# Performance work log

Measured on AMD Instinct MI355X. Metric: run time of the kernel, lower is better.

The kernel has to match this reference:

```python
import jax, jax.numpy as jnp
import numpy as np

B, T, I, H, O = 32, 128, 256, 512, 10


def setup_inputs() -> dict:
    key = jax.random.key(0)
    ks = jax.random.split(key, 16)
    s = 1.0 / np.sqrt(H)
    si = 1.0 / np.sqrt(I)
    inp = {
        "x": jax.random.normal(ks[0], (B, T, I), jnp.float32),
        # LSTM params (gate order: i, f, g, o)
        "Wih": jax.random.uniform(ks[1], (4 * H, I), jnp.float32, -si, si),
        "Whh": jax.random.uniform(ks[2], (4 * H, H), jnp.float32, -s, s),
        "b_lstm": jax.random.uniform(ks[3], (4 * H,), jnp.float32, -s, s),
        # readout dense
        "Wd": jax.random.uniform(ks[4], (O, H), jnp.float32, -s, s),
        "bd": jnp.zeros((O,), jnp.float32),
        # synthetic gradient MLP: H -> 512 -> 256 -> 128 -> H
        "Ws1": jax.random.uniform(ks[5], (512, H), jnp.float32, -s, s),
        "bs1": jnp.zeros((512,), jnp.float32),
        "Ws2": jax.random.uniform(ks[6], (256, 512), jnp.float32, -1.0 / np.sqrt(512), 1.0 / np.sqrt(512)),
        "bs2": jnp.zeros((256,), jnp.float32),
        "Ws3": jax.random.uniform(ks[7], (128, 256), jnp.float32, -1.0 / np.sqrt(256), 1.0 / np.sqrt(256)),
        "bs3": jnp.zeros((128,), jnp.float32),
        "Ws4": jax.random.uniform(ks[8], (H, 128), jnp.float32, -1.0 / np.sqrt(128), 1.0 / np.sqrt(128)),
        "bs4": jnp.zeros((H,), jnp.float32),
    }
    return inp


def reference(x, Wih, Whh, b_lstm, Wd, bd, Ws1, bs1, Ws2, bs2, Ws3, bs3, Ws4, bs4):
    # batch_first: [B,T,I] -> [T,B,I]
    xs = jnp.swapaxes(x, 0, 1)
    b, hid = x.shape[0], Whh.shape[1]

    h0 = jnp.zeros((b, hid), x.dtype)
    c0 = jnp.zeros((b, hid), x.dtype)
    # e-prop eligibility vectors: one row per (gate in {i,f,g}) x hidden unit
    ev_x0 = jnp.zeros((b, 3 * hid, Wih.shape[1]), x.dtype)
    ev_h0 = jnp.zeros((b, 3 * hid, hid), x.dtype)
    ev_b0 = jnp.zeros((b, 3 * hid, 1), x.dtype)

    def step(carry, xt):
        h, c, ev_x, ev_h, ev_b = carry
        gates = xt @ Wih.T + h @ Whh.T + b_lstm  # [B,4H]
        gi, gf, gg, go = jnp.split(gates, 4, axis=1)
        i = jax.nn.sigmoid(gi)
        f = jax.nn.sigmoid(gf)
        g = jnp.tanh(gg)
        o = jax.nn.sigmoid(go)
        # d(c_t)/d(pre-activation) for cell-affecting gates i, f, g  -> [B,3H]
        d = jnp.concatenate([g * i * (1.0 - i),
                             c * f * (1.0 - f),
                             i * (1.0 - g * g)], axis=1)
        f3 = jnp.concatenate([f, f, f], axis=1)  # forget-gate decay, tiled per gate
        # eligibility trace outer-product updates (the memory-bound core)
        ev_x_n = ev_x * f3[:, :, None] + d[:, :, None] * xt[:, None, :]
        ev_h_n = ev_h * f3[:, :, None] + d[:, :, None] * h[:, None, :]
        ev_b_n = ev_b * f3[:, :, None] + d[:, :, None]
        c_n = f * c + i * g
        h_n = o * jnp.tanh(c_n)
        return (h_n, c_n, ev_x_n, ev_h_n, ev_b_n), h_n

    (hT, cT, ev_x, ev_h, ev_b), hs = jax.lax.scan(step, (h0, c0, ev_x0, ev_h0, ev_b0), xs)

    last = hs[-1]  # [B,H]
    # synthetic gradient MLP on last hidden state
    z = jax.nn.relu(last @ Ws1.T + bs1)
    z = jax.nn.relu(z @ Ws2.T + bs2)
    z = jax.nn.relu(z @ Ws3.T + bs3)
    synth_grad = z @ Ws4.T + bs4  # [B,H]
    # readout on last hidden state (single_output=True)
    predictions = last @ Wd.T + bd  # [B,O]
    return (predictions, synth_grad, ev_x, ev_h, ev_b)
```

## Files before the change

kernel.cpp:

```cpp
#include <hip/hip_runtime.h>


typedef __attribute__((ext_vector_type(8))) short short8;
typedef __attribute__((ext_vector_type(4))) float f32x4;
typedef __attribute__((ext_vector_type(4))) unsigned u32x4;

#define DEV static __device__ __forceinline__

DEV unsigned f2bf(float x) {
  union { float f; unsigned u; } v; v.f = x;
  return (v.u + 0x7fffu + ((v.u >> 16) & 1u)) >> 16;
}
DEV float bf2f(unsigned b) {
  union { float f; unsigned u; } v; v.u = b << 16;
  return v.f;
}
struct HiLo { unsigned hi, lo; };
DEV HiLo packpair(float a, float b) {
  unsigned ha = f2bf(a), hb = f2bf(b);
  unsigned la = f2bf(a - bf2f(ha)), lb = f2bf(b - bf2f(hb));
  HiLo r; r.hi = ha | (hb << 16); r.lo = la | (lb << 16);
  return r;
}

#define SENT 0x7F7F7F7Fu

__global__ __launch_bounds__(1024) void lstm_rec(
    const float* __restrict__ Whh,
    const float* __restrict__ XW,
    unsigned* __restrict__ Hp,
    float* __restrict__ Hf,
    float* __restrict__ dh,
    float* __restrict__ fh)
{
  const int wg   = blockIdx.x;
  const int tid  = threadIdx.x;
  const int lane = tid & 63;
  const int wave = tid >> 6;
  const int tM   = wave & 1;
  const int tN   = wave >> 1;

  __shared__ __align__(16) unsigned Ldh[32 * 256];
  __shared__ float gl[32][132];

  const int cc = lane & 15;
  const int kb = lane >> 4;

  const int rloc  = tN * 16 + cc;
  const int jglob = (rloc >> 5) * 512 + wg * 32 + (rloc & 31);
  short8 whi[16];
#pragma unroll
  for (int s = 0; s < 16; ++s) {
    const float* wp = Whh + (size_t)jglob * 512 + s * 32 + kb * 8;
    f32x4 w0 = *(const f32x4*)wp;
    f32x4 w1 = *(const f32x4*)(wp + 4);
    short8 hi;
#pragma unroll
    for (int j = 0; j < 4; ++j) {
      hi[j]     = (short)f2bf(w0[j]);
      hi[4 + j] = (short)f2bf(w1[j]);
    }
    whi[s] = hi;
  }

  const int bA = tM * 16 + cc;
  const int mz = bA & 7;
  const unsigned rbase = (unsigned)(bA * 256 + ((kb ^ (mz & 3)) << 2) + ((mz >> 2) << 4));

  const int beW  = lane >> 1;
  const int half = lane & 1;
  const int swz  = beW & 7;
  const int C0   = wave * 4 + half * 2;

  const int be = tid >> 5;
  const int jo = tid & 31;
  const int jh = wg * 32 + jo;
  float c_reg = 0.f;

  for (int t = 0; t < 128; ++t) {
    const float* xwp = XW + (size_t)t * 65536 + (size_t)be * 2048 + wg * 32 + jo;
    float xwi = xwp[0], xwf = xwp[512], xwg = xwp[1024], xwo = xwp[1536];

    if (t > 0) {
      const unsigned* sp = Hp + ((size_t)t * 16 + wave) * 512 + lane * 8;
      u32x4 h0, h1;
      for (;;) {
#define SLICE_LOAD(dst, addr)                                          \
        asm volatile("global_load_dwordx4 %0, %1, off sc0 sc1"         \
                     : "=&v"(dst) : "v"(addr) : "memory")
        SLICE_LOAD(h0, sp);
        SLICE_LOAD(h1, sp + 4);
#undef SLICE_LOAD
        asm volatile("s_waitcnt vmcnt(0)" ::: "memory");
        __builtin_amdgcn_sched_barrier(0);
        unsigned bad = (unsigned)((h0[0] == SENT) | (h0[1] == SENT) |
                                  (h0[2] == SENT) | (h0[3] == SENT) |
                                  (h1[0] == SENT) | (h1[1] == SENT) |
                                  (h1[2] == SENT) | (h1[3] == SENT));
        if (!__any((int)bad)) break;
        __builtin_amdgcn_s_sleep(1);
      }
      __builtin_amdgcn_sched_barrier(0);

      const unsigned wb = (unsigned)(beW * 256);
      *(u32x4*)&Ldh[wb + (((C0 + 0) ^ swz) << 2)] = h0;
      *(u32x4*)&Ldh[wb + (((C0 + 1) ^ swz) << 2)] = h1;
    }
    __syncthreads();

    f32x4 acc;
    {
      f32x4 a0 = {0.f, 0.f, 0.f, 0.f}, a1 = a0;
      if (t > 0) {
#pragma unroll
        for (int s = 0; s < 16; s += 2) {
          const unsigned i0 = rbase ^ (unsigned)(s << 4);
          const unsigned i1 = rbase ^ (unsigned)((s + 1) << 4);
          short8 ah0 = __builtin_bit_cast(short8, *(const u32x4*)&Ldh[i0]);
          short8 ah1 = __builtin_bit_cast(short8, *(const u32x4*)&Ldh[i1]);
          a0 = __builtin_amdgcn_mfma_f32_16x16x32_bf16(ah0, whi[s],     a0, 0, 0, 0);
          a1 = __builtin_amdgcn_mfma_f32_16x16x32_bf16(ah1, whi[s + 1], a1, 0, 0, 0);
        }
      }
      acc = a0 + a1;
    }
#pragma unroll
    for (int r = 0; r < 4; ++r)
      gl[tM * 16 + kb * 4 + r][tN * 16 + cc] = acc[r];
    __syncthreads();

    {
      float pi = xwi + gl[be][jo];
      float pf = xwf + gl[be][32 + jo];
      float pg = xwg + gl[be][64 + jo];
      float po = xwo + gl[be][96 + jo];
      float ig = 1.f / (1.f + expf(-pi));
      float fg = 1.f / (1.f + expf(-pf));
      float gg = tanhf(pg);
      float og = 1.f / (1.f + expf(-po));
      float di = gg * ig * (1.f - ig);
      float df = c_reg * fg * (1.f - fg);
      float dg = ig * (1.f - gg * gg);
      c_reg = fg * c_reg + ig * gg;
      float hn = og * tanhf(c_reg);

      unsigned hh = f2bf(hn);
      unsigned hh_nb = (unsigned)__shfl_xor((int)hh, 1);
      if (!(jo & 1)) {
        unsigned stv = hh | (hh_nb << 16);
        size_t sa = ((size_t)(t + 1) * 16 + wg) * 512 + be * 16 + (jo >> 1);
        __hip_atomic_store(&Hp[sa], stv, __ATOMIC_RELAXED, __HIP_MEMORY_SCOPE_AGENT);
      }

      Hf[(size_t)(t + 1) * 16384 + (size_t)be * 512 + jh] = hn;
      size_t db = (size_t)t * 49152 + (size_t)be * 1536 + jh;
      dh[db] = di; dh[db + 512] = df; dh[db + 1024] = dg;
      fh[(size_t)t * 16384 + (size_t)be * 512 + jh] = fg;
    }
  }
}

__global__ __launch_bounds__(256) void suffix_A(
    float* __restrict__ dh, const float* __restrict__ fh,
    float* __restrict__ evb)
{
  const int g = blockIdx.x * 256 + threadIdx.x;
  const int b = g >> 9, jh = g & 511;
  float F = 1.f, s0 = 0.f, s1 = 0.f, s2 = 0.f;
  for (int t = 127; t >= 0; --t) {
    size_t db = (size_t)t * 49152 + (size_t)b * 1536 + jh;
    float a0 = dh[db] * F, a1 = dh[db + 512] * F, a2 = dh[db + 1024] * F;
    dh[db] = a0; dh[db + 512] = a1; dh[db + 1024] = a2;
    s0 += a0; s1 += a1; s2 += a2;
    F *= fh[(size_t)t * 16384 + (size_t)b * 512 + jh];
  }
  size_t eb = (size_t)b * 1536 + jh;
  evb[eb] = s0; evb[eb + 512] = s1; evb[eb + 1024] = s2;
}

__global__ __launch_bounds__(256, 2) void gemm_bf16s(
    const float* __restrict__ A, const float* __restrict__ B,
    float* __restrict__ C, const float* __restrict__ bias,
    int M, int N, int K,
    long long sAm, long long sAk, long long aBatch,
    long long sBn, long long sBk, long long bBatch,
    long long sCm1, long long sCm2, int M1, long long cBatch)
{
  __shared__ __align__(16) unsigned Ahi[128 * 20], Alo[128 * 20];
  __shared__ __align__(16) unsigned Bhi[128 * 20], Blo[128 * 20];

  const int tid  = threadIdx.x;
  const int lane = tid & 63;
  const int wave = tid >> 6;
  const int wm   = wave >> 1;
  const int wn   = wave & 1;
  const int cc   = lane & 15;
  const int kb   = lane >> 4;
  const long long z = blockIdx.z;
  const float* Ab = A + z * aBatch;
  const float* Bb = B + z * bBatch;
  const int m0 = blockIdx.y * 128, n0 = blockIdx.x * 128;

  f32x4 acc[4][4];
#pragma unroll
  for (int i = 0; i < 4; ++i)
#pragma unroll
    for (int j = 0; j < 4; ++j) acc[i][j] = (f32x4){0.f, 0.f, 0.f, 0.f};

  for (int k0 = 0; k0 < K; k0 += 32) {
    if (sAk == 1) {
      const int r = tid >> 1, half = tid & 1;
      const float* s = Ab + (long long)(m0 + r) * sAm + (k0 + half * 16);
      f32x4 v0 = *(const f32x4*)s;
      f32x4 v1 = *(const f32x4*)(s + 4);
      f32x4 v2 = *(const f32x4*)(s + 8);
      f32x4 v3 = *(const f32x4*)(s + 12);
      u32x4 h0, h1, l0, l1;
      HiLo p;
      p = packpair(v0[0], v0[1]); h0[0] = p.hi; l0[0] = p.lo;
      p = packpair(v0[2], v0[3]); h0[1] = p.hi; l0[1] = p.lo;
      p = packpair(v1[0], v1[1]); h0[2] = p.hi; l0[2] = p.lo;
      p = packpair(v1[2], v1[3]); h0[3] = p.hi; l0[3] = p.lo;
      p = packpair(v2[0], v2[1]); h1[0] = p.hi; l1[0] = p.lo;
      p = packpair(v2[2], v2[3]); h1[1] = p.hi; l1[1] = p.lo;
      p = packpair(v3[0], v3[1]); h1[2] = p.hi; l1[2] = p.lo;
      p = packpair(v3[2], v3[3]); h1[3] = p.hi; l1[3] = p.lo;
      const int o = r * 20 + half * 8;
      *(u32x4*)&Ahi[o] = h0;  *(u32x4*)&Ahi[o + 4] = h1;
      *(u32x4*)&Alo[o] = l0;  *(u32x4*)&Alo[o + 4] = l1;
    } else {
#pragma unroll
      for (int it = 0; it < 2; ++it) {
        const int kp = tid >> 4;
        const int mr = (tid & 15) * 4 + it * 64;
        const float* s0 = Ab + (long long)(k0 + 2 * kp) * sAk + (m0 + mr);
        f32x4 va = *(const f32x4*)s0;
        f32x4 vb = *(const f32x4*)(s0 + sAk);
#pragma unroll
        for (int q = 0; q < 4; ++q) {
          HiLo p = packpair(va[q], vb[q]);
          Ahi[(mr + q) * 20 + kp] = p.hi;
          Alo[(mr + q) * 20 + kp] = p.lo;
        }
      }
    }
    if (sBk == 1) {
      const int r = tid >> 1, half = tid & 1;
      const float* s = Bb + (long long)(n0 + r) * sBn + (k0 + half * 16);
      f32x4 v0 = *(const f32x4*)s;
      f32x4 v1 = *(const f32x4*)(s + 4);
      f32x4 v2 = *(const f32x4*)(s + 8);
      f32x4 v3 = *(const f32x4*)(s + 12);
      u32x4 h0, h1, l0, l1;
      HiLo p;
      p = packpair(v0[0], v0[1]); h0[0] = p.hi; l0[0] = p.lo;
      p = packpair(v0[2], v0[3]); h0[1] = p.hi; l0[1] = p.lo;
      p = packpair(v1[0], v1[1]); h0[2] = p.hi; l0[2] = p.lo;
      p = packpair(v1[2], v1[3]); h0[3] = p.hi; l0[3] = p.lo;
      p = packpair(v2[0], v2[1]); h1[0] = p.hi; l1[0] = p.lo;
      p = packpair(v2[2], v2[3]); h1[1] = p.hi; l1[1] = p.lo;
      p = packpair(v3[0], v3[1]); h1[2] = p.hi; l1[2] = p.lo;
      p = packpair(v3[2], v3[3]); h1[3] = p.hi; l1[3] = p.lo;
      const int o = r * 20 + half * 8;
      *(u32x4*)&Bhi[o] = h0;  *(u32x4*)&Bhi[o + 4] = h1;
      *(u32x4*)&Blo[o] = l0;  *(u32x4*)&Blo[o + 4] = l1;
    } else {
#pragma unroll
      for (int it = 0; it < 2; ++it) {
        const int kp = tid >> 4;
        const int nr = (tid & 15) * 4 + it * 64;
        const float* s0 = Bb + (long long)(k0 + 2 * kp) * sBk + (n0 + nr);
        f32x4 va = *(const f32x4*)s0;
        f32x4 vb = *(const f32x4*)(s0 + sBk);
#pragma unroll
        for (int q = 0; q < 4; ++q) {
          HiLo p = packpair(va[q], vb[q]);
          Bhi[(nr + q) * 20 + kp] = p.hi;
          Blo[(nr + q) * 20 + kp] = p.lo;
        }
      }
    }
    __syncthreads();

    short8 ah[4], al[4], bh[4], bl[4];
#pragma unroll
    for (int mi = 0; mi < 4; ++mi) {
      const int row = wm * 64 + mi * 16 + cc;
      ah[mi] = __builtin_bit_cast(short8, *(const u32x4*)&Ahi[row * 20 + kb * 4]);
      al[mi] = __builtin_bit_cast(short8, *(const u32x4*)&Alo[row * 20 + kb * 4]);
    }
#pragma unroll
    for (int ni = 0; ni < 4; ++ni) {
      const int row = wn * 64 + ni * 16 + cc;
      bh[ni] = __builtin_bit_cast(short8, *(const u32x4*)&Bhi[row * 20 + kb * 4]);
      bl[ni] = __builtin_bit_cast(short8, *(const u32x4*)&Blo[row * 20 + kb * 4]);
    }
#pragma unroll
    for (int mi = 0; mi < 4; ++mi)
#pragma unroll
      for (int ni = 0; ni < 4; ++ni) {
        acc[mi][ni] = __builtin_amdgcn_mfma_f32_16x16x32_bf16(ah[mi], bh[ni], acc[mi][ni], 0, 0, 0);
        acc[mi][ni] = __builtin_amdgcn_mfma_f32_16x16x32_bf16(ah[mi], bl[ni], acc[mi][ni], 0, 0, 0);
        acc[mi][ni] = __builtin_amdgcn_mfma_f32_16x16x32_bf16(al[mi], bh[ni], acc[mi][ni], 0, 0, 0);
      }
    __syncthreads();
  }

#pragma unroll
  for (int ni = 0; ni < 4; ++ni) {
    const int ng = n0 + wn * 64 + ni * 16 + cc;
    const float bv = bias ? bias[ng] : 0.f;
#pragma unroll
    for (int mi = 0; mi < 4; ++mi) {
#pragma unroll
      for (int r = 0; r < 4; ++r) {
        const int mg = m0 + wm * 64 + mi * 16 + kb * 4 + r;
        const long long crow = z * cBatch + (long long)(mg % M1) * sCm1 +
                               (long long)(mg / M1) * sCm2;
        C[crow + ng] = acc[mi][ni][r] + bv;
      }
    }
  }
}

template <int BM, int BN, int TM, int TN>
__global__ __launch_bounds__(256) void gemm_f32(
    const float* __restrict__ A, const float* __restrict__ B,
    float* __restrict__ C, const float* __restrict__ bias,
    int M, int N, int K,
    long long sAm, long long sAk, long long aBatch,
    long long sBn, long long sBk, long long bBatch,
    long long sCm1, long long sCm2, int M1, long long cBatch,
    int relu)
{
  constexpr int BK = 16;
  __shared__ float As[BK][BM + 4];
  __shared__ float Bs[BK][BN + 4];
  const int tid = threadIdx.x;
  const long long z = blockIdx.z;
  const float* Ab = A + z * aBatch;
  const float* Bb = B + z * bBatch;
  const int m0 = blockIdx.y * BM, n0 = blockIdx.x * BN;
  constexpr int tn_cnt = BN / TN;
  const int tm0 = (tid / tn_cnt) * TM;
  const int tn0 = (tid % tn_cnt) * TN;

  float acc[TM][TN];
#pragma unroll
  for (int i = 0; i < TM; ++i)
#pragma unroll
    for (int j = 0; j < TN; ++j) acc[i][j] = 0.f;

  for (int k0 = 0; k0 < K; k0 += BK) {
    if (sAk == 1) {
      for (int m = tid >> 2; m < BM; m += 64) {
        const int kq = (tid & 3) * 4;
        f32x4 v = {0.f, 0.f, 0.f, 0.f};
        if (m0 + m < M) v = *(const f32x4*)(Ab + (long long)(m0 + m) * sAm + (k0 + kq));
        As[kq + 0][m] = v[0]; As[kq + 1][m] = v[1];
        As[kq + 2][m] = v[2]; As[kq + 3][m] = v[3];
      }
    } else {
      constexpr int mq_cnt = BM / 4;
      for (int kk = tid / mq_cnt; kk < BK; kk += 256 / mq_cnt) {
        const int mq = (tid % mq_cnt) * 4;
        f32x4 v = {0.f, 0.f, 0.f, 0.f};
        if (m0 + mq < M) v = *(const f32x4*)(Ab + (long long)(k0 + kk) * sAk + (m0 + mq));
        *(f32x4*)&As[kk][mq] = v;
      }
    }
    if (sBk == 1) {
      for (int n = tid >> 2; n < BN; n += 64) {
        const int kq = (tid & 3) * 4;
        f32x4 v = {0.f, 0.f, 0.f, 0.f};
        if (n0 + n < N) v = *(const f32x4*)(Bb + (long long)(n0 + n) * sBn + (k0 + kq));
        Bs[kq + 0][n] = v[0]; Bs[kq + 1][n] = v[1];
        Bs[kq + 2][n] = v[2]; Bs[kq + 3][n] = v[3];
      }
    } else {
      constexpr int nq_cnt = BN / 4;
      for (int kk = tid / nq_cnt; kk < BK; kk += 256 / nq_cnt) {
        const int nq = (tid % nq_cnt) * 4;
        f32x4 v = {0.f, 0.f, 0.f, 0.f};
        if (n0 + nq < N) v = *(const f32x4*)(Bb + (long long)(k0 + kk) * sBk + (n0 + nq));
        *(f32x4*)&Bs[kk][nq] = v;
      }
    }
    __syncthreads();

#pragma unroll
    for (int kk = 0; kk < BK; ++kk) {
      float a[TM], bb[TN];
#pragma unroll
      for (int i = 0; i < TM; ++i) a[i] = As[kk][tm0 + i];
#pragma unroll
      for (int j = 0; j < TN; ++j) bb[j] = Bs[kk][tn0 + j];
#pragma unroll
      for (int i = 0; i < TM; ++i)
#pragma unroll
        for (int j = 0; j < TN; ++j) acc[i][j] += a[i] * bb[j];
    }
    __syncthreads();
  }

#pragma unroll
  for (int i = 0; i < TM; ++i) {
    const int mg = m0 + tm0 + i;
    if (mg >= M) continue;
    const long long crow = z * cBatch + (long long)(mg % M1) * sCm1 +
                           (long long)(mg / M1) * sCm2;
#pragma unroll
    for (int j = 0; j < TN; ++j) {
      const int ng = n0 + tn0 + j;
      if (ng >= N) continue;
      float v = acc[i][j];
      if (bias) v += bias[ng];
      if (relu) v = fmaxf(v, 0.f);
      C[crow + ng] = v;
    }
  }
}

extern "C" void kernel_launch(void* const* d_in, const int* in_sizes, int n_in,
                              void* d_out, int out_size, void* d_ws, size_t ws_size,
                              hipStream_t stream) {
  const float* x   = (const float*)d_in[0];
  const float* Wih = (const float*)d_in[1];
  const float* Whh = (const float*)d_in[2];
  const float* bl  = (const float*)d_in[3];
  const float* Wd  = (const float*)d_in[4];
  const float* bd  = (const float*)d_in[5];
  const float* Ws1 = (const float*)d_in[6];
  const float* bs1 = (const float*)d_in[7];
  const float* Ws2 = (const float*)d_in[8];
  const float* bs2 = (const float*)d_in[9];
  const float* Ws3 = (const float*)d_in[10];
  const float* bs3 = (const float*)d_in[11];
  const float* Ws4 = (const float*)d_in[12];
  const float* bs4 = (const float*)d_in[13];

  float* out = (float*)d_out;
  float* ws  = (float*)d_ws;

  const long long OP = 0, OS = 320, OEX = 16704, OEH = 12599616, OEB = 37765440;

  float* XW = out + OEH;
  float* fh = out + OEH + 8388608;
  unsigned* Hp = (unsigned*)(out + OEH + 10485760);

  float* dh = ws;
  float* Hf = ws + 6291456;
  float* z1 = ws + 8404992;
  float* z2 = ws + 8421376;
  float* z3 = ws + 8429568;

  hipMemsetAsync(Hp, 0x7F, 129ull * 16 * 512 * sizeof(unsigned), stream);
  hipMemsetAsync(Hf, 0, 16384 * sizeof(float), stream);

  dim3 blk(256);

  gemm_bf16s<<<dim3(16, 32, 1), blk, 0, stream>>>(
      x, Wih, XW, bl, 4096, 2048, 256,
      256, 1, 0,
      256, 1, 0,
      65536, 2048, 128, 0);

  lstm_rec<<<dim3(16), dim3(1024), 0, stream>>>(Whh, XW, Hp, Hf, dh, fh);

  suffix_A<<<dim3(64), blk, 0, stream>>>(dh, fh, out + OEB);

  const float* hlast = Hf + 2097152;
  gemm_f32<32, 32, 2, 2><<<dim3(16, 1, 1), blk, 0, stream>>>(
      hlast, Ws1, z1, bs1, 32, 512, 512, 512, 1, 0, 512, 1, 0, 512, 0, 32, 0, 1);
  gemm_f32<32, 32, 2, 2><<<dim3(8, 1, 1), blk, 0, stream>>>(
      z1, Ws2, z2, bs2, 32, 256, 512, 512, 1, 0, 512, 1, 0, 256, 0, 32, 0, 1);
  gemm_f32<32, 32, 2, 2><<<dim3(4, 1, 1), blk, 0, stream>>>(
      z2, Ws3, z3, bs3, 32, 128, 256, 256, 1, 0, 256, 1, 0, 128, 0, 32, 0, 1);
  gemm_f32<32, 32, 2, 2><<<dim3(16, 1, 1), blk, 0, stream>>>(
      z3, Ws4, out + OS, bs4, 32, 512, 128, 128, 1, 0, 128, 1, 0, 512, 0, 32, 0, 0);
  gemm_f32<32, 32, 2, 2><<<dim3(1, 1, 1), blk, 0, stream>>>(
      hlast, Wd, out + OP, bd, 32, 10, 512, 512, 1, 0, 512, 1, 0, 10, 0, 32, 0, 0);

  gemm_bf16s<<<dim3(2, 12, 32), blk, 0, stream>>>(
      dh, x, out + OEX, nullptr, 1536, 256, 128,
      1, 49152, 1536,
      1, 256, 32768,
      256, 0, 1536, 393216);

  gemm_bf16s<<<dim3(4, 12, 32), blk, 0, stream>>>(
      dh, Hf, out + OEH, nullptr, 1536, 512, 128,
      1, 49152, 1536,
      1, 16384, 512,
      512, 0, 1536, 786432);
}
```

Baseline: 775.9 us.

## Halve LSTM recurrence block size, give each wave two gate tiles

Result: faster. 677.8 us (-12.6%).

```diff
diff --git a/kernel.cpp b/kernel.cpp
--- a/kernel.cpp
+++ b/kernel.cpp
@@ -2,6 +2,7 @@
 
 
 typedef __attribute__((ext_vector_type(8))) short short8;
+typedef __attribute__((ext_vector_type(2))) float f32x2;
 typedef __attribute__((ext_vector_type(4))) float f32x4;
 typedef __attribute__((ext_vector_type(4))) unsigned u32x4;
 
@@ -25,7 +26,7 @@
 
 #define SENT 0x7F7F7F7Fu
 
-__global__ __launch_bounds__(1024) void lstm_rec(
+__global__ __launch_bounds__(512, 2) void lstm_rec(
     const float* __restrict__ Whh,
     const float* __restrict__ XW,
     unsigned* __restrict__ Hp,
@@ -46,21 +47,24 @@
   const int cc = lane & 15;
   const int kb = lane >> 4;
 
-  const int rloc  = tN * 16 + cc;
-  const int jglob = (rloc >> 5) * 512 + wg * 32 + (rloc & 31);
-  short8 whi[16];
-#pragma unroll
-  for (int s = 0; s < 16; ++s) {
-    const float* wp = Whh + (size_t)jglob * 512 + s * 32 + kb * 8;
-    f32x4 w0 = *(const f32x4*)wp;
-    f32x4 w1 = *(const f32x4*)(wp + 4);
-    short8 hi;
-#pragma unroll
-    for (int j = 0; j < 4; ++j) {
-      hi[j]     = (short)f2bf(w0[j]);
-      hi[4 + j] = (short)f2bf(w1[j]);
-    }
-    whi[s] = hi;
+  short8 whiA[16], whiB[16];
+#pragma unroll
+  for (int q = 0; q < 2; ++q) {
+    const int rloc  = (tN * 2 + q) * 16 + cc;
+    const int jglob = (rloc >> 5) * 512 + wg * 32 + (rloc & 31);
+#pragma unroll
+    for (int s = 0; s < 16; ++s) {
+      const float* wp = Whh + (size_t)jglob * 512 + s * 32 + kb * 8;
+      f32x4 w0 = *(const f32x4*)wp;
+      f32x4 w1 = *(const f32x4*)(wp + 4);
+      short8 hi;
+#pragma unroll
+      for (int j = 0; j < 4; ++j) {
+        hi[j]     = (short)f2bf(w0[j]);
+        hi[4 + j] = (short)f2bf(w1[j]);
+      }
+      if (q == 0) whiA[s] = hi; else whiB[s] = hi;
+    }
   }
 
   const int bA = tM * 16 + cc;
@@ -70,92 +74,100 @@
   const int beW  = lane >> 1;
   const int half = lane & 1;
   const int swz  = beW & 7;
-  const int C0   = wave * 4 + half * 2;
-
-  const int be = tid >> 5;
-  const int jo = tid & 31;
-  const int jh = wg * 32 + jo;
-  float c_reg = 0.f;
+  const int Ca   = 4 * (wave * 2)     + half * 2;
+  const int Cb   = 4 * (wave * 2 + 1) + half * 2;
+
+  const int be  = tid >> 4;
+  const int jo0 = (tid & 15) * 2;
+  const int jh0 = wg * 32 + jo0;
+  float c0 = 0.f, c1 = 0.f;
 
   for (int t = 0; t < 128; ++t) {
-    const float* xwp = XW + (size_t)t * 65536 + (size_t)be * 2048 + wg * 32 + jo;
-    float xwi = xwp[0], xwf = xwp[512], xwg = xwp[1024], xwo = xwp[1536];
+    const float* xwp = XW + (size_t)t * 65536 + (size_t)be * 2048 + wg * 32 + jo0;
+    f32x2 xwi = *(const f32x2*)(xwp);
+    f32x2 xwf = *(const f32x2*)(xwp + 512);
+    f32x2 xwg = *(const f32x2*)(xwp + 1024);
+    f32x2 xwo = *(const f32x2*)(xwp + 1536);
 
     if (t > 0) {
-      const unsigned* sp = Hp + ((size_t)t * 16 + wave) * 512 + lane * 8;
-      u32x4 h0, h1;
+      const unsigned* sp0 = Hp + ((size_t)t * 16 + wave * 2) * 512 + lane * 8;
+      const unsigned* sp1 = sp0 + 512;
+      u32x4 a0, a1, b0, b1;
       for (;;) {
 #define SLICE_LOAD(dst, addr)                                          \
         asm volatile("global_load_dwordx4 %0, %1, off sc0 sc1"         \
                      : "=&v"(dst) : "v"(addr) : "memory")
-        SLICE_LOAD(h0, sp);
-        SLICE_LOAD(h1, sp + 4);
+        SLICE_LOAD(a0, sp0);
+        SLICE_LOAD(a1, sp0 + 4);
+        SLICE_LOAD(b0, sp1);
+        SLICE_LOAD(b1, sp1 + 4);
 #undef SLICE_LOAD
         asm volatile("s_waitcnt vmcnt(0)" ::: "memory");
         __builtin_amdgcn_sched_barrier(0);
-        unsigned bad = (unsigned)((h0[0] == SENT) | (h0[1] == SENT) |
-                                  (h0[2] == SENT) | (h0[3] == SENT) |
-                                  (h1[0] == SENT) | (h1[1] == SENT) |
-                                  (h1[2] == SENT) | (h1[3] == SENT));
+        unsigned bad = (unsigned)((a0[0] == SENT) | (a0[1] == SENT) |
+                                  (a0[2] == SENT) | (a0[3] == SENT) |
+                                  (a1[0] == SENT) | (a1[1] == SENT) |
+                                  (a1[2] == SENT) | (a1[3] == SENT) |
+                                  (b0[0] == SENT) | (b0[1] == SENT) |
+                                  (b0[2] == SENT) | (b0[3] == SENT) |
+                                  (b1[0] == SENT) | (b1[1] == SENT) |
+                                  (b1[2] == SENT) | (b1[3] == SENT));
         if (!__any((int)bad)) break;
         __builtin_amdgcn_s_sleep(1);
       }
       __builtin_amdgcn_sched_barrier(0);
 
       const unsigned wb = (unsigned)(beW * 256);
-      *(u32x4*)&Ldh[wb + (((C0 + 0) ^ swz) << 2)] = h0;
-      *(u32x4*)&Ldh[wb + (((C0 + 1) ^ swz) << 2)] = h1;
+      *(u32x4*)&Ldh[wb + (((Ca + 0) ^ swz) << 2)] = a0;
+      *(u32x4*)&Ldh[wb + (((Ca + 1) ^ swz) << 2)] = a1;
+      *(u32x4*)&Ldh[wb + (((Cb + 0) ^ swz) << 2)] = b0;
+      *(u32x4*)&Ldh[wb + (((Cb + 1) ^ swz) << 2)] = b1;
     }
     __syncthreads();
 
-    f32x4 acc;
+    f32x4 acc0 = {0.f, 0.f, 0.f, 0.f}, acc1 = acc0;
+    if (t > 0) {
+#pragma unroll
+      for (int s = 0; s < 16; ++s) {
+        const unsigned idx = rbase ^ (unsigned)(s << 4);
+        short8 ah = __builtin_bit_cast(short8, *(const u32x4*)&Ldh[idx]);
+        acc0 = __builtin_amdgcn_mfma_f32_16x16x32_bf16(ah, whiA[s], acc0, 0, 0, 0);
+        acc1 = __builtin_amdgcn_mfma_f32_16x16x32_bf16(ah, whiB[s], acc1, 0, 0, 0);
+      }
+    }
+#pragma unroll
+    for (int r = 0; r < 4; ++r) {
+      gl[tM * 16 + kb * 4 + r][(tN * 2 + 0) * 16 + cc] = acc0[r];
+      gl[tM * 16 + kb * 4 + r][(tN * 2 + 1) * 16 + cc] = acc1[r];
+    }
+    __syncthreads();
+
     {
-      f32x4 a0 = {0.f, 0.f, 0.f, 0.f}, a1 = a0;
-      if (t > 0) {
-#pragma unroll
-        for (int s = 0; s < 16; s += 2) {
-          const unsigned i0 = rbase ^ (unsigned)(s << 4);
-          const unsigned i1 = rbase ^ (unsigned)((s + 1) << 4);
-          short8 ah0 = __builtin_bit_cast(short8, *(const u32x4*)&Ldh[i0]);
-          short8 ah1 = __builtin_bit_cast(short8, *(const u32x4*)&Ldh[i1]);
-          a0 = __builtin_amdgcn_mfma_f32_16x16x32_bf16(ah0, whi[s],     a0, 0, 0, 0);
-          a1 = __builtin_amdgcn_mfma_f32_16x16x32_bf16(ah1, whi[s + 1], a1, 0, 0, 0);
-        }
-      }
-      acc = a0 + a1;
-    }
-#pragma unroll
-    for (int r = 0; r < 4; ++r)
-      gl[tM * 16 + kb * 4 + r][tN * 16 + cc] = acc[r];
-    __syncthreads();
-
-    {
-      float pi = xwi + gl[be][jo];
-      float pf = xwf + gl[be][32 + jo];
-      float pg = xwg + gl[be][64 + jo];
-      float po = xwo + gl[be][96 + jo];
-      float ig = 1.f / (1.f + expf(-pi));
-      float fg = 1.f / (1.f + expf(-pf));
-      float gg = tanhf(pg);
-      float og = 1.f / (1.f + expf(-po));
-      float di = gg * ig * (1.f - ig);
-      float df = c_reg * fg * (1.f - fg);
-      float dg = ig * (1.f - gg * gg);
-      c_reg = fg * c_reg + ig * gg;
-      float hn = og * tanhf(c_reg);
-
-      unsigned hh = f2bf(hn);
-      unsigned hh_nb = (unsigned)__shfl_xor((int)hh, 1);
-      if (!(jo & 1)) {
-        unsigned stv = hh | (hh_nb << 16);
-        size_t sa = ((size_t)(t + 1) * 16 + wg) * 512 + be * 16 + (jo >> 1);
-        __hip_atomic_store(&Hp[sa], stv, __ATOMIC_RELAXED, __HIP_MEMORY_SCOPE_AGENT);
-      }
-
-      Hf[(size_t)(t + 1) * 16384 + (size_t)be * 512 + jh] = hn;
-      size_t db = (size_t)t * 49152 + (size_t)be * 1536 + jh;
-      dh[db] = di; dh[db + 512] = df; dh[db + 1024] = dg;
-      fh[(size_t)t * 16384 + (size_t)be * 512 + jh] = fg;
+      float pi0 = xwi[0] + gl[be][jo0],       pi1 = xwi[1] + gl[be][jo0 + 1];
+      float pf0 = xwf[0] + gl[be][32 + jo0],  pf1 = xwf[1] + gl[be][33 + jo0];
+      float pg0 = xwg[0] + gl[be][64 + jo0],  pg1 = xwg[1] + gl[be][65 + jo0];
+      float po0 = xwo[0] + gl[be][96 + jo0],  po1 = xwo[1] + gl[be][97 + jo0];
+      float ig0 = 1.f / (1.f + expf(-pi0)),   ig1 = 1.f / (1.f + expf(-pi1));
+      float fg0 = 1.f / (1.f + expf(-pf0)),   fg1 = 1.f / (1.f + expf(-pf1));
+      float gg0 = tanhf(pg0),                 gg1 = tanhf(pg1);
+      float og0 = 1.f / (1.f + expf(-po0)),   og1 = 1.f / (1.f + expf(-po1));
+      float di0 = gg0 * ig0 * (1.f - ig0),    di1 = gg1 * ig1 * (1.f - ig1);
+      float df0 = c0 * fg0 * (1.f - fg0),     df1 = c1 * fg1 * (1.f - fg1);
+      float dg0 = ig0 * (1.f - gg0 * gg0),    dg1 = ig1 * (1.f - gg1 * gg1);
+      c0 = fg0 * c0 + ig0 * gg0;              c1 = fg1 * c1 + ig1 * gg1;
+      float h0 = og0 * tanhf(c0),             h1 = og1 * tanhf(c1);
+
+      unsigned stv = f2bf(h0) | (f2bf(h1) << 16);
+      size_t sa = ((size_t)(t + 1) * 16 + wg) * 512 + be * 16 + (jo0 >> 1);
+      __hip_atomic_store(&Hp[sa], stv, __ATOMIC_RELAXED, __HIP_MEMORY_SCOPE_AGENT);
+
+      size_t ho = (size_t)(t + 1) * 16384 + (size_t)be * 512 + jh0;
+      *(f32x2*)&Hf[ho] = (f32x2){h0, h1};
+      size_t db = (size_t)t * 49152 + (size_t)be * 1536 + jh0;
+      *(f32x2*)&dh[db]        = (f32x2){di0, di1};
+      *(f32x2*)&dh[db + 512]  = (f32x2){df0, df1};
+      *(f32x2*)&dh[db + 1024] = (f32x2){dg0, dg1};
+      *(f32x2*)&fh[(size_t)t * 16384 + (size_t)be * 512 + jh0] = (f32x2){fg0, fg1};
     }
   }
 }
@@ -465,7 +477,7 @@
       256, 1, 0,
       65536, 2048, 128, 0);
 
-  lstm_rec<<<dim3(16), dim3(1024), 0, stream>>>(Whh, XW, Hp, Hf, dh, fh);
+  lstm_rec<<<dim3(16), dim3(512), 0, stream>>>(Whh, XW, Hp, Hf, dh, fh);
 
   suffix_A<<<dim3(64), blk, 0, stream>>>(dh, fh, out + OEB);
 
```
